# Optimization experiments

Measured on AMD Instinct MI355X. Metric: run time of the kernel, lower is better.

The kernel has to match this reference:

```python
import jax, jax.numpy as jnp
import numpy as np

N = 512     # nodes
E = 16384   # edges (N * avg_degree 32, unique pairs)
F = 64      # nedgeinput
FO = 64     # nedgeoutput


def setup_inputs() -> dict:
    key = jax.random.key(0)
    ks = jax.random.split(key, 7)
    # unique edge pairs so scatter-assign is well-defined
    perm = jax.random.permutation(ks[0], N * N)[:E]
    edge_index = jnp.stack([perm // N, perm % N]).astype(jnp.int32)  # [2, E]
    C = jax.random.normal(ks[1], (E, F), dtype=jnp.float32)
    batch_node = jax.random.normal(ks[2], (N,), dtype=jnp.float32)
    s = 1.0 / np.sqrt(F)
    W_L1 = jax.random.normal(ks[3], (F, F), dtype=jnp.float32) * s          # Linear(F, F), weight [out,in]
    W_L2 = jax.random.normal(ks[4], (F, F), dtype=jnp.float32) * s
    W_mlp1 = jax.random.normal(ks[5], (8 * F, 2 * F), dtype=jnp.float32) * (1.0 / np.sqrt(2 * F))
    W_mlp2 = jax.random.normal(ks[6], (FO, 8 * F), dtype=jnp.float32) * (1.0 / np.sqrt(8 * F))
    return {"edge_index": edge_index, "C": C, "batch_node": batch_node,
            "W_L1": W_L1, "W_L2": W_L2, "W_mlp1": W_mlp1, "W_mlp2": W_mlp2}


def reference(edge_index, C, batch_node, W_L1, W_L2, W_mlp1, W_mlp2):
    n = batch_node.shape[0]
    f = C.shape[1]
    ei0, ei1 = edge_index[0], edge_index[1]
    X = C @ W_L1.T  # [E, F]  (L1(C))
    Y = C @ W_L2.T  # [E, F]  (L2(C))
    # scatter edges into dense [F, N, N] adjacency-like tensors
    resx = jnp.zeros((f, n, n), dtype=C.dtype).at[:, ei0, ei1].set(X.T)
    resy = jnp.zeros((f, n, n), dtype=C.dtype).at[:, ei0, ei1].set(Y.T)
    # batched dense matmul per feature channel, then gather back at edges
    res = jnp.einsum('fij,fjk->fik', resx, resy)  # [F, N, N]
    tmp_matmul = res[:, ei0, ei1].T  # [E, F]
    tmp = jnp.concatenate([C, tmp_matmul], axis=1)  # [E, 2F]
    return jax.nn.relu(tmp @ W_mlp1.T) @ W_mlp2.T  # [E, FO]
```

## Files before the change

kernel.cpp:

```cpp
#include <hip/hip_runtime.h>

#define NN 512
#define NE 16384
#define NF 64

typedef __attribute__((ext_vector_type(8))) short short8_t;
typedef __attribute__((ext_vector_type(4))) float float4_t;

__device__ inline unsigned short f2bf(float f) {
  unsigned u = __builtin_bit_cast(unsigned, f);
  u += 0x7fff + ((u >> 16) & 1);
  return (unsigned short)(u >> 16);
}
__device__ inline float bf2f(unsigned short u) {
  unsigned v = ((unsigned)u) << 16;
  return __builtin_bit_cast(float, v);
}

__global__ __launch_bounds__(256) void k_xy_mfma(const float* __restrict__ C,
                                                 const float* __restrict__ W1,
                                                 const float* __restrict__ W2,
                                                 const int* __restrict__ ei,
                                                 const float* __restrict__ Wm1,
                                                 const float* __restrict__ Wm2,
                                                 int* __restrict__ eid,
                                                 unsigned* __restrict__ maskO,
                                                 unsigned* __restrict__ maskI,
                                                 unsigned short* __restrict__ Xb,
                                                 unsigned short* __restrict__ Yb,
                                                 unsigned short* __restrict__ W1B,
                                                 unsigned short* __restrict__ W2B) {
  __shared__ __attribute__((aligned(16))) short W1s[64 * 72];
  __shared__ __attribute__((aligned(16))) short W2s[64 * 72];
  int t = threadIdx.x;
  int w = t >> 6;
  int lane = t & 63;
  int col = lane & 15;
  int q = lane >> 4;
  int base_e = blockIdx.x * 64 + w * 16;

  if (t < 64) {
    int e = blockIdx.x * 64 + t;
    int i = ei[e];
    int k = ei[NE + e];
    eid[i * NN + k] = e;
    atomicOr(&maskO[i * 16 + (k >> 5)], 1u << (k & 31));
    atomicOr(&maskI[k * 16 + (i >> 5)], 1u << (i & 31));
  }

  if (t >= 64 && t < 160) {
    int t4 = blockIdx.x * 96 + (t - 64);
    if (t4 < 16384) {
      float4 v = ((const float4*)Wm1)[t4];
      short4 s;
      s.x = f2bf(v.x); s.y = f2bf(v.y); s.z = f2bf(v.z); s.w = f2bf(v.w);
      ((short4*)W1B)[t4] = s;
    } else {
      int i2 = t4 - 16384;
      float4 v = ((const float4*)Wm2)[i2];
      short4 s;
      s.x = f2bf(v.x); s.y = f2bf(v.y); s.z = f2bf(v.z); s.w = f2bf(v.w);
      ((short4*)W2B)[i2] = s;
    }
  }

#pragma unroll
  for (int z = 0; z < 4; z++) {
    int gi = z * 256 + t;
    int r = gi >> 4, c = gi & 15;
    float4 v1 = ((const float4*)W1)[r * 16 + c];
    float4 v2 = ((const float4*)W2)[r * 16 + c];
    short4 s1, s2;
    s1.x = f2bf(v1.x); s1.y = f2bf(v1.y); s1.z = f2bf(v1.z); s1.w = f2bf(v1.w);
    s2.x = f2bf(v2.x); s2.y = f2bf(v2.y); s2.z = f2bf(v2.z); s2.w = f2bf(v2.w);
    *(short4*)(W1s + r * 72 + c * 4) = s1;
    *(short4*)(W2s + r * 72 + c * 4) = s2;
  }
  __syncthreads();

  short8_t bfrag[2];
#pragma unroll
  for (int ks = 0; ks < 2; ks++) {
    float4 c0 = ((const float4*)C)[(size_t)(base_e + col) * 16 + ks * 8 + q * 2];
    float4 c1 = ((const float4*)C)[(size_t)(base_e + col) * 16 + ks * 8 + q * 2 + 1];
    short8_t s;
    s[0] = (short)f2bf(c0.x); s[1] = (short)f2bf(c0.y);
    s[2] = (short)f2bf(c0.z); s[3] = (short)f2bf(c0.w);
    s[4] = (short)f2bf(c1.x); s[5] = (short)f2bf(c1.y);
    s[6] = (short)f2bf(c1.z); s[7] = (short)f2bf(c1.w);
    bfrag[ks] = s;
  }

  float4_t xa[4], ya[4];
#pragma unroll
  for (int ft = 0; ft < 4; ft++) {
    xa[ft] = (float4_t){0.f, 0.f, 0.f, 0.f};
    ya[ft] = (float4_t){0.f, 0.f, 0.f, 0.f};
  }
#pragma unroll
  for (int ks = 0; ks < 2; ks++) {
#pragma unroll
    for (int ft = 0; ft < 4; ft++) {
      short8_t a1 = *(const short8_t*)(W1s + (ft * 16 + col) * 72 + ks * 32 + q * 8);
      short8_t a2 = *(const short8_t*)(W2s + (ft * 16 + col) * 72 + ks * 32 + q * 8);
      xa[ft] = __builtin_amdgcn_mfma_f32_16x16x32_bf16(a1, bfrag[ks], xa[ft], 0, 0, 0);
      ya[ft] = __builtin_amdgcn_mfma_f32_16x16x32_bf16(a2, bfrag[ks], ya[ft], 0, 0, 0);
    }
  }
#pragma unroll
  for (int ft = 0; ft < 4; ft++) {
    short4 sx, sy;
    sx.x = (short)f2bf(xa[ft][0]); sx.y = (short)f2bf(xa[ft][1]);
    sx.z = (short)f2bf(xa[ft][2]); sx.w = (short)f2bf(xa[ft][3]);
    sy.x = (short)f2bf(ya[ft][0]); sy.y = (short)f2bf(ya[ft][1]);
    sy.z = (short)f2bf(ya[ft][2]); sy.w = (short)f2bf(ya[ft][3]);
    *(short4*)(Xb + (size_t)(base_e + col) * 64 + ft * 16 + q * 4) = sx;
    *(short4*)(Yb + (size_t)(base_e + col) * 64 + ft * 16 + q * 4) = sy;
  }
}

#define STAGE(it) { \
    uint4* d1 = (uint4*)W1s; const uint4* s1g = (const uint4*)W1B; \
    _Pragma("unroll") for (int z = 0; z < 4; z++) { \
      int gi = z * 512 + t; int r = gi >> 4, c = gi & 15; \
      int grow = ((r >> 6) * 4 + (it)) * 64 + (r & 63); \
      d1[r * 17 + c] = s1g[(size_t)grow * 16 + c]; } \
    uint4* d2 = (uint4*)W2s; const uint4* s2g = (const uint4*)W2B; \
    _Pragma("unroll") for (int z = 0; z < 2; z++) { \
      int gi = z * 512 + t; int r = gi >> 4, c = gi & 15; \
      int gc = ((c >> 3) * 4 + (it)) * 8 + (c & 7); \
      d2[r * 17 + c] = s2g[(size_t)r * 64 + gc]; } }

#define REMBATCH(le, ii, kk, cnt, ac) { \
    int t2 = base + b; \
    int jj = jlbase[(le) * 32 + (t2 < (cnt) ? t2 : base)] & 511; \
    int sv = eid[(gl < 8) ? ((ii) * NN + jj) : (jj * NN + (kk))]; \
    short4 xs[8], ys[8]; \
    _Pragma("unroll") for (int b2 = 0; b2 < 8; b2++) { \
      int s1 = __shfl(sv, (lane & 48) | b2); \
      int s2 = __shfl(sv, (lane & 48) | (8 + b2)); \
      xs[b2] = *(const short4*)(Xb + (size_t)s1 * 64 + gl * 4); \
      ys[b2] = *(const short4*)(Yb + (size_t)s2 * 64 + gl * 4); } \
    _Pragma("unroll") for (int b2 = 0; b2 < 8; b2++) if (base + b2 < (cnt)) { \
      ac[0] = fmaf(bf2f((unsigned short)xs[b2].x), bf2f((unsigned short)ys[b2].x), ac[0]); \
      ac[1] = fmaf(bf2f((unsigned short)xs[b2].y), bf2f((unsigned short)ys[b2].y), ac[1]); \
      ac[2] = fmaf(bf2f((unsigned short)xs[b2].z), bf2f((unsigned short)ys[b2].z), ac[2]); \
      ac[3] = fmaf(bf2f((unsigned short)xs[b2].w), bf2f((unsigned short)ys[b2].w), ac[3]); } }

__global__ __launch_bounds__(512) void k_spmlp(
    const int* __restrict__ ei,
    const int* __restrict__ eid,
    const unsigned* __restrict__ maskO,
    const unsigned* __restrict__ maskI,
    const unsigned short* __restrict__ Xb,
    const unsigned short* __restrict__ Yb,
    const float* __restrict__ C,
    const unsigned short* __restrict__ W1B,
    const unsigned short* __restrict__ W2B,
    float* __restrict__ out) {
  __shared__ __attribute__((aligned(16))) short W1s[128 * 136];
  __shared__ __attribute__((aligned(16))) short W2s[64 * 136];
  __shared__ __attribute__((aligned(16))) short hS[8][16 * 72];
  __shared__ __attribute__((aligned(16))) short tm[64 * 72];

  int t = threadIdx.x;
  int w = t >> 6;
  int lane = t & 63;
  int gl = lane & 15;
  int grp = lane >> 4;
  unsigned short* jlbase = (unsigned short*)hS;

  int u = w >> 2;
  int wl = w & 3;
  int g = wl & 1;
  int h = wl >> 1;
  int col = lane & 15;
  int q = lane >> 4;
  int base_e = blockIdx.x * 64 + u * 32 + g * 16;
  int lem = u * 32 + g * 16 + col;

  int le0 = w * 4 + grp;
  int le1 = 32 + w * 4 + grp;
  int e0 = blockIdx.x * 64 + le0;
  int e1 = blockIdx.x * 64 + le1;
  int i0 = ei[e0], k0 = ei[NE + e0];
  int i1 = ei[e1], k1 = ei[NE + e1];

  float4 craw[4];
#pragma unroll
  for (int ks = 0; ks < 2; ks++) {
    craw[2 * ks]     = ((const float4*)C)[(size_t)(base_e + col) * 16 + ks * 8 + q * 2];
    craw[2 * ks + 1] = ((const float4*)C)[(size_t)(base_e + col) * 16 + ks * 8 + q * 2 + 1];
  }
  STAGE(0);

  unsigned mm0 = maskO[i0 * 16 + gl] & maskI[k0 * 16 + gl];
  unsigned mm1 = maskO[i1 * 16 + gl] & maskI[k1 * 16 + gl];

  int cnt0, cnt1;
#pragma unroll
  for (int round = 0; round < 2; round++) {
    unsigned mm = round ? mm1 : mm0;
    int le = round ? le1 : le0;
    int mcnt = __popc(mm);
    int incl = mcnt;
#pragma unroll
    for (int d = 1; d < 16; d <<= 1) {
      int y = __shfl(incl, (lane & 48) | ((gl - d) & 15));
      if (gl >= d) incl += y;
    }
    int off = incl - mcnt;
    int cnt = __shfl(incl, (lane & 48) | 15);
    unsigned bits = mm;
    while (bits) {
      int bb = __builtin_ctz(bits);
      bits &= bits - 1;
      if (off < 32) jlbase[le * 32 + off] = (unsigned short)(gl * 32 + bb);
      off++;
    }
    if (cnt > 32) cnt = 32;
    if (round) cnt1 = cnt; else cnt0 = cnt;
  }

  int b = gl & 7;
  float ac0[4] = {0.f, 0.f, 0.f, 0.f}, ac1[4] = {0.f, 0.f, 0.f, 0.f};
  {
    int jj0 = jlbase[le0 * 32 + (b < cnt0 ? b : 0)] & 511;
    int jj1 = jlbase[le1 * 32 + (b < cnt1 ? b : 0)] & 511;
    int sv0 = (cnt0 > 0) ? eid[(gl < 8) ? (i0 * NN + jj0) : (jj0 * NN + k0)] : 0;
    int sv1 = (cnt1 > 0) ? eid[(gl < 8) ? (i1 * NN + jj1) : (jj1 * NN + k1)] : 0;
    short4 xs0[8], ys0[8], xs1[8], ys1[8];
#pragma unroll
    for (int b2 = 0; b2 < 8; b2++) {
      int s1 = __shfl(sv0, (lane & 48) | b2);
      int s2 = __shfl(sv0, (lane & 48) | (8 + b2));
      xs0[b2] = *(const short4*)(Xb + (size_t)s1 * 64 + gl * 4);
      ys0[b2] = *(const short4*)(Yb + (size_t)s2 * 64 + gl * 4);
    }
#pragma unroll
    for (int b2 = 0; b2 < 8; b2++) {
      int s1 = __shfl(sv1, (lane & 48) | b2);
      int s2 = __shfl(sv1, (lane & 48) | (8 + b2));
      xs1[b2] = *(const short4*)(Xb + (size_t)s1 * 64 + gl * 4);
      ys1[b2] = *(const short4*)(Yb + (size_t)s2 * 64 + gl * 4);
    }
#pragma unroll
    for (int b2 = 0; b2 < 8; b2++) if (b2 < cnt0) {
      ac0[0] = fmaf(bf2f((unsigned short)xs0[b2].x), bf2f((unsigned short)ys0[b2].x), ac0[0]);
      ac0[1] = fmaf(bf2f((unsigned short)xs0[b2].y), bf2f((unsigned short)ys0[b2].y), ac0[1]);
      ac0[2] = fmaf(bf2f((unsigned short)xs0[b2].z), bf2f((unsigned short)ys0[b2].z), ac0[2]);
      ac0[3] = fmaf(bf2f((unsigned short)xs0[b2].w), bf2f((unsigned short)ys0[b2].w), ac0[3]);
    }
#pragma unroll
    for (int b2 = 0; b2 < 8; b2++) if (b2 < cnt1) {
      ac1[0] = fmaf(bf2f((unsigned short)xs1[b2].x), bf2f((unsigned short)ys1[b2].x), ac1[0]);
      ac1[1] = fmaf(bf2f((unsigned short)xs1[b2].y), bf2f((unsigned short)ys1[b2].y), ac1[1]);
      ac1[2] = fmaf(bf2f((unsigned short)xs1[b2].z), bf2f((unsigned short)ys1[b2].z), ac1[2]);
      ac1[3] = fmaf(bf2f((unsigned short)xs1[b2].w), bf2f((unsigned short)ys1[b2].w), ac1[3]);
    }
  }
  for (int base = 8; base < cnt0; base += 8) REMBATCH(le0, i0, k0, cnt0, ac0);
  for (int base = 8; base < cnt1; base += 8) REMBATCH(le1, i1, k1, cnt1, ac1);

  {
    short4 o0, o1;
    o0.x = (short)f2bf(ac0[0]); o0.y = (short)f2bf(ac0[1]);
    o0.z = (short)f2bf(ac0[2]); o0.w = (short)f2bf(ac0[3]);
    o1.x = (short)f2bf(ac1[0]); o1.y = (short)f2bf(ac1[1]);
    o1.z = (short)f2bf(ac1[2]); o1.w = (short)f2bf(ac1[3]);
    *(short4*)(tm + le0 * 72 + gl * 4) = o0;
    *(short4*)(tm + le1 * 72 + gl * 4) = o1;
  }

  __syncthreads();

  short8_t btmp[4];
#pragma unroll
  for (int ks = 0; ks < 2; ks++) {
    float4 c0 = craw[2 * ks], c1 = craw[2 * ks + 1];
    short8_t s;
    s[0] = (short)f2bf(c0.x); s[1] = (short)f2bf(c0.y);
    s[2] = (short)f2bf(c0.z); s[3] = (short)f2bf(c0.w);
    s[4] = (short)f2bf(c1.x); s[5] = (short)f2bf(c1.y);
    s[6] = (short)f2bf(c1.z); s[7] = (short)f2bf(c1.w);
    btmp[ks] = s;
  }
#pragma unroll
  for (int ks = 2; ks < 4; ks++)
    btmp[ks] = *(const short8_t*)(tm + lem * 72 + (ks - 2) * 32 + q * 8);

  float4_t oacc[4];
#pragma unroll
  for (int ft = 0; ft < 4; ft++) oacc[ft] = (float4_t){0.f, 0.f, 0.f, 0.f};

  for (int it = 0; it < 4; it++) {
#pragma unroll
    for (int ht = 0; ht < 4; ht++) {
      float4_t hacc = (float4_t){0.f, 0.f, 0.f, 0.f};
#pragma unroll
      for (int ks = 0; ks < 4; ks++) {
        short8_t af = *(const short8_t*)(W1s + (h * 64 + ht * 16 + col) * 136 + ks * 32 + q * 8);
        hacc = __builtin_amdgcn_mfma_f32_16x16x32_bf16(af, btmp[ks], hacc, 0, 0, 0);
      }
      short4 hp;
      hp.x = (short)f2bf(fmaxf(hacc[0], 0.f));
      hp.y = (short)f2bf(fmaxf(hacc[1], 0.f));
      hp.z = (short)f2bf(fmaxf(hacc[2], 0.f));
      hp.w = (short)f2bf(fmaxf(hacc[3], 0.f));
      *(short4*)(&hS[w][col * 72 + ht * 16 + q * 4]) = hp;
    }

#pragma unroll
    for (int ks2 = 0; ks2 < 2; ks2++) {
      short8_t a2 = *(const short8_t*)(&hS[w][col * 72 + ks2 * 32 + q * 8]);
#pragma unroll
      for (int ft = 0; ft < 4; ft++) {
        short8_t b2 = *(const short8_t*)(W2s + (ft * 16 + col) * 136 + h * 64 + ks2 * 32 + q * 8);
        oacc[ft] = __builtin_amdgcn_mfma_f32_16x16x32_bf16(a2, b2, oacc[ft], 0, 0, 0);
      }
    }

    if (it < 3) {
      __syncthreads();
      STAGE(it + 1);
      __syncthreads();
    }
  }

  __syncthreads();
  float* red = (float*)W1s;
  if (h == 1) {
#pragma unroll
    for (int ft = 0; ft < 4; ft++)
#pragma unroll
      for (int r = 0; r < 4; r++)
        red[(u * 32 + g * 16 + q * 4 + r) * 66 + ft * 16 + col] = oacc[ft][r];
  }
  __syncthreads();
  if (h == 0) {
#pragma unroll
    for (int ft = 0; ft < 4; ft++)
#pragma unroll
      for (int r = 0; r < 4; r++) {
        float v = oacc[ft][r] + red[(u * 32 + g * 16 + q * 4 + r) * 66 + ft * 16 + col];
        out[(size_t)(base_e + q * 4 + r) * 64 + ft * 16 + col] = v;
      }
  }
}

extern "C" void kernel_launch(void* const* d_in, const int* in_sizes, int n_in,
                              void* d_out, int out_size, void* d_ws, size_t ws_size,
                              hipStream_t stream) {
  const int* ei = (const int*)d_in[0];
  const float* C = (const float*)d_in[1];
  const float* W1 = (const float*)d_in[3];
  const float* W2 = (const float*)d_in[4];
  const float* Wm1 = (const float*)d_in[5];
  const float* Wm2 = (const float*)d_in[6];
  float* out = (float*)d_out;

  char* p = (char*)d_ws;
  int* eid = (int*)p;                 p += (size_t)NN * NN * 4;
  unsigned* masks = (unsigned*)p;     p += (size_t)16384 * 4;
  unsigned short* Xb = (unsigned short*)p;    p += (size_t)NE * NF * 2;
  unsigned short* Yb = (unsigned short*)p;    p += (size_t)NE * NF * 2;
  unsigned short* W1B = (unsigned short*)p;   p += (size_t)512 * 128 * 2;
  unsigned short* W2B = (unsigned short*)p;   p += (size_t)64 * 512 * 2;
  unsigned* maskO = masks;
  unsigned* maskI = masks + 8192;

  hipMemsetAsync(masks, 0, 16384 * sizeof(unsigned), stream);
  k_xy_mfma<<<NE / 64, 256, 0, stream>>>(C, W1, W2, ei, Wm1, Wm2, eid,
                                         maskO, maskI, Xb, Yb, W1B, W2B);
  k_spmlp<<<NE / 64, 512, 0, stream>>>(ei, eid, maskO, maskI, Xb, Yb,
                                       C, W1B, W2B, out);
}
```

Measured before the change: 88.34 us.

## Fuse projection and sparse-MLP kernels into one cooperative kernel with grid sync

Merges the X/Y projection kernel and the sparse matmul+MLP kernel into a single cooperative launch of 256 blocks, separated by a grid-wide barrier. The global memset and scattered global atomics for the adjacency bitmasks are replaced by two blocks that each build one full mask in shared memory with LDS atomics and then copy it out. This removes a kernel launch, the memset, and global atomic traffic. In exchange, two blocks serially scan all 16384 edges with 128 threads, which can lengthen the critical path before the grid sync. It also raises shared memory use and relies on all 256 blocks being co-resident.

```diff
diff --git a/kernel.cpp b/kernel.cpp
--- a/kernel.cpp
+++ b/kernel.cpp
@@ -1,8 +1,11 @@
 #include <hip/hip_runtime.h>
+#include <hip/hip_cooperative_groups.h>
 
 #define NN 512
 #define NE 16384
 #define NF 64
+
+namespace cg = cooperative_groups;
 
 typedef __attribute__((ext_vector_type(8))) short short8_t;
 typedef __attribute__((ext_vector_type(4))) float float4_t;
@@ -15,108 +18,6 @@
 __device__ inline float bf2f(unsigned short u) {
   unsigned v = ((unsigned)u) << 16;
   return __builtin_bit_cast(float, v);
-}
-
-__global__ __launch_bounds__(256) void k_xy_mfma(const float* __restrict__ C,
-                                                 const float* __restrict__ W1,
-                                                 const float* __restrict__ W2,
-                                                 const int* __restrict__ ei,
-                                                 const float* __restrict__ Wm1,
-                                                 const float* __restrict__ Wm2,
-                                                 int* __restrict__ eid,
-                                                 unsigned* __restrict__ maskO,
-                                                 unsigned* __restrict__ maskI,
-                                                 unsigned short* __restrict__ Xb,
-                                                 unsigned short* __restrict__ Yb,
-                                                 unsigned short* __restrict__ W1B,
-                                                 unsigned short* __restrict__ W2B) {
-  __shared__ __attribute__((aligned(16))) short W1s[64 * 72];
-  __shared__ __attribute__((aligned(16))) short W2s[64 * 72];
-  int t = threadIdx.x;
-  int w = t >> 6;
-  int lane = t & 63;
-  int col = lane & 15;
-  int q = lane >> 4;
-  int base_e = blockIdx.x * 64 + w * 16;
-
-  if (t < 64) {
-    int e = blockIdx.x * 64 + t;
-    int i = ei[e];
-    int k = ei[NE + e];
-    eid[i * NN + k] = e;
-    atomicOr(&maskO[i * 16 + (k >> 5)], 1u << (k & 31));
-    atomicOr(&maskI[k * 16 + (i >> 5)], 1u << (i & 31));
-  }
-
-  if (t >= 64 && t < 160) {
-    int t4 = blockIdx.x * 96 + (t - 64);
-    if (t4 < 16384) {
-      float4 v = ((const float4*)Wm1)[t4];
-      short4 s;
-      s.x = f2bf(v.x); s.y = f2bf(v.y); s.z = f2bf(v.z); s.w = f2bf(v.w);
-      ((short4*)W1B)[t4] = s;
-    } else {
-      int i2 = t4 - 16384;
-      float4 v = ((const float4*)Wm2)[i2];
-      short4 s;
-      s.x = f2bf(v.x); s.y = f2bf(v.y); s.z = f2bf(v.z); s.w = f2bf(v.w);
-      ((short4*)W2B)[i2] = s;
-    }
-  }
-
-#pragma unroll
-  for (int z = 0; z < 4; z++) {
-    int gi = z * 256 + t;
-    int r = gi >> 4, c = gi & 15;
-    float4 v1 = ((const float4*)W1)[r * 16 + c];
-    float4 v2 = ((const float4*)W2)[r * 16 + c];
-    short4 s1, s2;
-    s1.x = f2bf(v1.x); s1.y = f2bf(v1.y); s1.z = f2bf(v1.z); s1.w = f2bf(v1.w);
-    s2.x = f2bf(v2.x); s2.y = f2bf(v2.y); s2.z = f2bf(v2.z); s2.w = f2bf(v2.w);
-    *(short4*)(W1s + r * 72 + c * 4) = s1;
-    *(short4*)(W2s + r * 72 + c * 4) = s2;
-  }
-  __syncthreads();
-
-  short8_t bfrag[2];
-#pragma unroll
-  for (int ks = 0; ks < 2; ks++) {
-    float4 c0 = ((const float4*)C)[(size_t)(base_e + col) * 16 + ks * 8 + q * 2];
-    float4 c1 = ((const float4*)C)[(size_t)(base_e + col) * 16 + ks * 8 + q * 2 + 1];
-    short8_t s;
-    s[0] = (short)f2bf(c0.x); s[1] = (short)f2bf(c0.y);
-    s[2] = (short)f2bf(c0.z); s[3] = (short)f2bf(c0.w);
-    s[4] = (short)f2bf(c1.x); s[5] = (short)f2bf(c1.y);
-    s[6] = (short)f2bf(c1.z); s[7] = (short)f2bf(c1.w);
-    bfrag[ks] = s;
-  }
-
-  float4_t xa[4], ya[4];
-#pragma unroll
-  for (int ft = 0; ft < 4; ft++) {
-    xa[ft] = (float4_t){0.f, 0.f, 0.f, 0.f};
-    ya[ft] = (float4_t){0.f, 0.f, 0.f, 0.f};
-  }
-#pragma unroll
-  for (int ks = 0; ks < 2; ks++) {
-#pragma unroll
-    for (int ft = 0; ft < 4; ft++) {
-      short8_t a1 = *(const short8_t*)(W1s + (ft * 16 + col) * 72 + ks * 32 + q * 8);
-      short8_t a2 = *(const short8_t*)(W2s + (ft * 16 + col) * 72 + ks * 32 + q * 8);
-      xa[ft] = __builtin_amdgcn_mfma_f32_16x16x32_bf16(a1, bfrag[ks], xa[ft], 0, 0, 0);
-      ya[ft] = __builtin_amdgcn_mfma_f32_16x16x32_bf16(a2, bfrag[ks], ya[ft], 0, 0, 0);
-    }
-  }
-#pragma unroll
-  for (int ft = 0; ft < 4; ft++) {
-    short4 sx, sy;
-    sx.x = (short)f2bf(xa[ft][0]); sx.y = (short)f2bf(xa[ft][1]);
-    sx.z = (short)f2bf(xa[ft][2]); sx.w = (short)f2bf(xa[ft][3]);
-    sy.x = (short)f2bf(ya[ft][0]); sy.y = (short)f2bf(ya[ft][1]);
-    sy.z = (short)f2bf(ya[ft][2]); sy.w = (short)f2bf(ya[ft][3]);
-    *(short4*)(Xb + (size_t)(base_e + col) * 64 + ft * 16 + q * 4) = sx;
-    *(short4*)(Yb + (size_t)(base_e + col) * 64 + ft * 16 + q * 4) = sy;
-  }
 }
 
 #define STAGE(it) { \
@@ -147,21 +48,26 @@
       ac[2] = fmaf(bf2f((unsigned short)xs[b2].z), bf2f((unsigned short)ys[b2].z), ac[2]); \
       ac[3] = fmaf(bf2f((unsigned short)xs[b2].w), bf2f((unsigned short)ys[b2].w), ac[3]); } }
 
-__global__ __launch_bounds__(512) void k_spmlp(
+__global__ __launch_bounds__(512) void k_mega(
     const int* __restrict__ ei,
-    const int* __restrict__ eid,
-    const unsigned* __restrict__ maskO,
-    const unsigned* __restrict__ maskI,
-    const unsigned short* __restrict__ Xb,
-    const unsigned short* __restrict__ Yb,
     const float* __restrict__ C,
-    const unsigned short* __restrict__ W1B,
-    const unsigned short* __restrict__ W2B,
+    const float* __restrict__ W1,
+    const float* __restrict__ W2,
+    const float* __restrict__ Wm1,
+    const float* __restrict__ Wm2,
+    int* __restrict__ eid,
+    unsigned* __restrict__ maskO,
+    unsigned* __restrict__ maskI,
+    unsigned short* __restrict__ Xb,
+    unsigned short* __restrict__ Yb,
+    unsigned short* __restrict__ W1B,
+    unsigned short* __restrict__ W2B,
     float* __restrict__ out) {
   __shared__ __attribute__((aligned(16))) short W1s[128 * 136];
   __shared__ __attribute__((aligned(16))) short W2s[64 * 136];
   __shared__ __attribute__((aligned(16))) short hS[8][16 * 72];
   __shared__ __attribute__((aligned(16))) short tm[64 * 72];
+  __shared__ unsigned mlds[8192];
 
   int t = threadIdx.x;
   int w = t >> 6;
@@ -169,6 +75,8 @@
   int gl = lane & 15;
   int grp = lane >> 4;
   unsigned short* jlbase = (unsigned short*)hS;
+  short* k1W1s = &hS[0][0];
+  short* k1W2s = k1W1s + 64 * 72;
 
   int u = w >> 2;
   int wl = w & 3;
@@ -192,6 +100,112 @@
     craw[2 * ks]     = ((const float4*)C)[(size_t)(base_e + col) * 16 + ks * 8 + q * 2];
     craw[2 * ks + 1] = ((const float4*)C)[(size_t)(base_e + col) * 16 + ks * 8 + q * 2 + 1];
   }
+
+  if (blockIdx.x < 2) {
+    uint4 z4 = {0u, 0u, 0u, 0u};
+#pragma unroll
+    for (int z = 0; z < 4; z++) ((uint4*)mlds)[t * 4 + z] = z4;
+  }
+
+  if (t < 256) {
+#pragma unroll
+    for (int z = 0; z < 4; z++) {
+      int gi = z * 256 + t;
+      int r = gi >> 4, c = gi & 15;
+      float4 v1 = ((const float4*)W1)[r * 16 + c];
+      float4 v2 = ((const float4*)W2)[r * 16 + c];
+      short4 s1, s2;
+      s1.x = f2bf(v1.x); s1.y = f2bf(v1.y); s1.z = f2bf(v1.z); s1.w = f2bf(v1.w);
+      s2.x = f2bf(v2.x); s2.y = f2bf(v2.y); s2.z = f2bf(v2.z); s2.w = f2bf(v2.w);
+      *(short4*)(k1W1s + r * 72 + c * 4) = s1;
+      *(short4*)(k1W2s + r * 72 + c * 4) = s2;
+    }
+  } else if (t < 352) {
+    int t4 = blockIdx.x * 96 + (t - 256);
+    if (t4 < 16384) {
+      float4 v = ((const float4*)Wm1)[t4];
+      short4 s;
+      s.x = f2bf(v.x); s.y = f2bf(v.y); s.z = f2bf(v.z); s.w = f2bf(v.w);
+      ((short4*)W1B)[t4] = s;
+    } else {
+      int i2 = t4 - 16384;
+      float4 v = ((const float4*)Wm2)[i2];
+      short4 s;
+      s.x = f2bf(v.x); s.y = f2bf(v.y); s.z = f2bf(v.z); s.w = f2bf(v.w);
+      ((short4*)W2B)[i2] = s;
+    }
+  }
+
+  if (t < 64) {
+    int e = blockIdx.x * 64 + t;
+    eid[ei[e] * NN + ei[NE + e]] = e;
+  }
+
+  __syncthreads();
+
+  if (t < 256) {
+    int be = blockIdx.x * 64 + w * 16;
+    short8_t bfrag[2];
+#pragma unroll
+    for (int ks = 0; ks < 2; ks++) {
+      float4 c0 = ((const float4*)C)[(size_t)(be + col) * 16 + ks * 8 + q * 2];
+      float4 c1 = ((const float4*)C)[(size_t)(be + col) * 16 + ks * 8 + q * 2 + 1];
+      short8_t s;
+      s[0] = (short)f2bf(c0.x); s[1] = (short)f2bf(c0.y);
+      s[2] = (short)f2bf(c0.z); s[3] = (short)f2bf(c0.w);
+      s[4] = (short)f2bf(c1.x); s[5] = (short)f2bf(c1.y);
+      s[6] = (short)f2bf(c1.z); s[7] = (short)f2bf(c1.w);
+      bfrag[ks] = s;
+    }
+    float4_t xa[4], ya[4];
+#pragma unroll
+    for (int ft = 0; ft < 4; ft++) {
+      xa[ft] = (float4_t){0.f, 0.f, 0.f, 0.f};
+      ya[ft] = (float4_t){0.f, 0.f, 0.f, 0.f};
+    }
+#pragma unroll
+    for (int ks = 0; ks < 2; ks++) {
+#pragma unroll
+      for (int ft = 0; ft < 4; ft++) {
+        short8_t a1 = *(const short8_t*)(k1W1s + (ft * 16 + col) * 72 + ks * 32 + q * 8);
+        short8_t a2 = *(const short8_t*)(k1W2s + (ft * 16 + col) * 72 + ks * 32 + q * 8);
+        xa[ft] = __builtin_amdgcn_mfma_f32_16x16x32_bf16(a1, bfrag[ks], xa[ft], 0, 0, 0);
+        ya[ft] = __builtin_amdgcn_mfma_f32_16x16x32_bf16(a2, bfrag[ks], ya[ft], 0, 0, 0);
+      }
+    }
+#pragma unroll
+    for (int ft = 0; ft < 4; ft++) {
+      short4 sx, sy;
+      sx.x = (short)f2bf(xa[ft][0]); sx.y = (short)f2bf(xa[ft][1]);
+      sx.z = (short)f2bf(xa[ft][2]); sx.w = (short)f2bf(xa[ft][3]);
+      sy.x = (short)f2bf(ya[ft][0]); sy.y = (short)f2bf(ya[ft][1]);
+      sy.z = (short)f2bf(ya[ft][2]); sy.w = (short)f2bf(ya[ft][3]);
+      *(short4*)(Xb + (size_t)(be + col) * 64 + ft * 16 + q * 4) = sx;
+      *(short4*)(Yb + (size_t)(be + col) * 64 + ft * 16 + q * 4) = sy;
+    }
+  } else if (t >= 384 && blockIdx.x == 0) {
+    for (int e = t - 384; e < NE; e += 128) {
+      int ii = ei[e], kk = ei[NE + e];
+      atomicOr(&mlds[ii * 16 + (kk >> 5)], 1u << (kk & 31));
+    }
+  } else if (t >= 384 && blockIdx.x == 1) {
+    for (int e = t - 384; e < NE; e += 128) {
+      int ii = ei[e], kk = ei[NE + e];
+      atomicOr(&mlds[kk * 16 + (ii >> 5)], 1u << (ii & 31));
+    }
+  }
+
+  if (blockIdx.x < 2) {
+    __syncthreads();
+    unsigned* dst = (blockIdx.x == 0) ? maskO : maskI;
+#pragma unroll
+    for (int z = 0; z < 4; z++)
+      ((uint4*)dst)[t * 4 + z] = ((const uint4*)mlds)[t * 4 + z];
+  }
+
+  __threadfence();
+  cg::this_grid().sync();
+
   STAGE(0);
 
   unsigned mm0 = maskO[i0 * 16 + gl] & maskI[k0 * 16 + gl];
@@ -369,9 +383,10 @@
   unsigned* maskO = masks;
   unsigned* maskI = masks + 8192;
 
-  hipMemsetAsync(masks, 0, 16384 * sizeof(unsigned), stream);
-  k_xy_mfma<<<NE / 64, 256, 0, stream>>>(C, W1, W2, ei, Wm1, Wm2, eid,
-                                         maskO, maskI, Xb, Yb, W1B, W2B);
-  k_spmlp<<<NE / 64, 512, 0, stream>>>(ei, eid, maskO, maskI, Xb, Yb,
-                                       C, W1B, W2B, out);
+  void* args[] = {(void*)&ei, (void*)&C, (void*)&W1, (void*)&W2,
+                  (void*)&Wm1, (void*)&Wm2, (void*)&eid, (void*)&maskO,
+                  (void*)&maskI, (void*)&Xb, (void*)&Yb, (void*)&W1B,
+                  (void*)&W2B, (void*)&out};
+  hipLaunchCooperativeKernel((const void*)k_mega, dim3(256), dim3(512),
+                             args, 0, stream);
 }
```

New measurement: 218.3 us. +147.1%, slower.

## Double-buffer MLP weight staging and split X/Y projection across more blocks

Applied to the files above, without the earlier changes.

The MLP kernel now holds its weight tiles in two LDS buffers. The next slice is loaded into registers before compute and written to the other buffer afterwards, so global weight loads overlap the MFMA work and each iteration needs one barrier instead of two. The projection kernel gives each wave either X or Y for 16 edges and launches twice as many blocks with 32 edges each, hoisting the C loads to the top. Double buffering doubles the weight LDS footprint, which may reduce occupancy.

```diff
diff --git a/kernel.cpp b/kernel.cpp
--- a/kernel.cpp
+++ b/kernel.cpp
@@ -37,10 +37,19 @@
   int lane = t & 63;
   int col = lane & 15;
   int q = lane >> 4;
-  int base_e = blockIdx.x * 64 + w * 16;
-
-  if (t < 64) {
-    int e = blockIdx.x * 64 + t;
+  int p = w >> 1;
+  int xy = w & 1;
+  int base_e = blockIdx.x * 32 + p * 16;
+
+  float4 c0[2], c1[2];
+#pragma unroll
+  for (int ks = 0; ks < 2; ks++) {
+    c0[ks] = ((const float4*)C)[(size_t)(base_e + col) * 16 + ks * 8 + q * 2];
+    c1[ks] = ((const float4*)C)[(size_t)(base_e + col) * 16 + ks * 8 + q * 2 + 1];
+  }
+
+  if (t < 32) {
+    int e = blockIdx.x * 32 + t;
     int i = ei[e];
     int k = ei[NE + e];
     eid[i * NN + k] = e;
@@ -48,8 +57,8 @@
     atomicOr(&maskI[k * 16 + (i >> 5)], 1u << (i & 31));
   }
 
-  if (t >= 64 && t < 160) {
-    int t4 = blockIdx.x * 96 + (t - 64);
+  if (t >= 64 && t < 112) {
+    int t4 = blockIdx.x * 48 + (t - 64);
     if (t4 < 16384) {
       float4 v = ((const float4*)Wm1)[t4];
       short4 s;
@@ -81,55 +90,57 @@
   short8_t bfrag[2];
 #pragma unroll
   for (int ks = 0; ks < 2; ks++) {
-    float4 c0 = ((const float4*)C)[(size_t)(base_e + col) * 16 + ks * 8 + q * 2];
-    float4 c1 = ((const float4*)C)[(size_t)(base_e + col) * 16 + ks * 8 + q * 2 + 1];
     short8_t s;
-    s[0] = (short)f2bf(c0.x); s[1] = (short)f2bf(c0.y);
-    s[2] = (short)f2bf(c0.z); s[3] = (short)f2bf(c0.w);
-    s[4] = (short)f2bf(c1.x); s[5] = (short)f2bf(c1.y);
-    s[6] = (short)f2bf(c1.z); s[7] = (short)f2bf(c1.w);
+    s[0] = (short)f2bf(c0[ks].x); s[1] = (short)f2bf(c0[ks].y);
+    s[2] = (short)f2bf(c0[ks].z); s[3] = (short)f2bf(c0[ks].w);
+    s[4] = (short)f2bf(c1[ks].x); s[5] = (short)f2bf(c1[ks].y);
+    s[6] = (short)f2bf(c1[ks].z); s[7] = (short)f2bf(c1[ks].w);
     bfrag[ks] = s;
   }
 
-  float4_t xa[4], ya[4];
+  const short* Ws = xy ? W2s : W1s;
+  unsigned short* Ob = xy ? Yb : Xb;
+  float4_t acc[4];
+#pragma unroll
+  for (int ft = 0; ft < 4; ft++) acc[ft] = (float4_t){0.f, 0.f, 0.f, 0.f};
+#pragma unroll
+  for (int ks = 0; ks < 2; ks++) {
+#pragma unroll
+    for (int ft = 0; ft < 4; ft++) {
+      short8_t a = *(const short8_t*)(Ws + (ft * 16 + col) * 72 + ks * 32 + q * 8);
+      acc[ft] = __builtin_amdgcn_mfma_f32_16x16x32_bf16(a, bfrag[ks], acc[ft], 0, 0, 0);
+    }
+  }
 #pragma unroll
   for (int ft = 0; ft < 4; ft++) {
-    xa[ft] = (float4_t){0.f, 0.f, 0.f, 0.f};
-    ya[ft] = (float4_t){0.f, 0.f, 0.f, 0.f};
-  }
-#pragma unroll
-  for (int ks = 0; ks < 2; ks++) {
-#pragma unroll
-    for (int ft = 0; ft < 4; ft++) {
-      short8_t a1 = *(const short8_t*)(W1s + (ft * 16 + col) * 72 + ks * 32 + q * 8);
-      short8_t a2 = *(const short8_t*)(W2s + (ft * 16 + col) * 72 + ks * 32 + q * 8);
-      xa[ft] = __builtin_amdgcn_mfma_f32_16x16x32_bf16(a1, bfrag[ks], xa[ft], 0, 0, 0);
-      ya[ft] = __builtin_amdgcn_mfma_f32_16x16x32_bf16(a2, bfrag[ks], ya[ft], 0, 0, 0);
-    }
-  }
-#pragma unroll
-  for (int ft = 0; ft < 4; ft++) {
-    short4 sx, sy;
-    sx.x = (short)f2bf(xa[ft][0]); sx.y = (short)f2bf(xa[ft][1]);
-    sx.z = (short)f2bf(xa[ft][2]); sx.w = (short)f2bf(xa[ft][3]);
-    sy.x = (short)f2bf(ya[ft][0]); sy.y = (short)f2bf(ya[ft][1]);
-    sy.z = (short)f2bf(ya[ft][2]); sy.w = (short)f2bf(ya[ft][3]);
-    *(short4*)(Xb + (size_t)(base_e + col) * 64 + ft * 16 + q * 4) = sx;
-    *(short4*)(Yb + (size_t)(base_e + col) * 64 + ft * 16 + q * 4) = sy;
-  }
-}
-
-#define STAGE(it) { \
-    uint4* d1 = (uint4*)W1s; const uint4* s1g = (const uint4*)W1B; \
+    short4 so;
+    so.x = (short)f2bf(acc[ft][0]); so.y = (short)f2bf(acc[ft][1]);
+    so.z = (short)f2bf(acc[ft][2]); so.w = (short)f2bf(acc[ft][3]);
+    *(short4*)(Ob + (size_t)(base_e + col) * 64 + ft * 16 + q * 4) = so;
+  }
+}
+
+#define STAGE_LOAD(it, r1, r2) { \
+    const uint4* s1g = (const uint4*)W1B; \
     _Pragma("unroll") for (int z = 0; z < 4; z++) { \
       int gi = z * 512 + t; int r = gi >> 4, c = gi & 15; \
       int grow = ((r >> 6) * 4 + (it)) * 64 + (r & 63); \
-      d1[r * 17 + c] = s1g[(size_t)grow * 16 + c]; } \
-    uint4* d2 = (uint4*)W2s; const uint4* s2g = (const uint4*)W2B; \
+      r1[z] = s1g[(size_t)grow * 16 + c]; } \
+    const uint4* s2g = (const uint4*)W2B; \
     _Pragma("unroll") for (int z = 0; z < 2; z++) { \
       int gi = z * 512 + t; int r = gi >> 4, c = gi & 15; \
       int gc = ((c >> 3) * 4 + (it)) * 8 + (c & 7); \
-      d2[r * 17 + c] = s2g[(size_t)r * 64 + gc]; } }
+      r2[z] = s2g[(size_t)r * 64 + gc]; } }
+
+#define STAGE_WRITE(buf, r1, r2) { \
+    uint4* d1 = (uint4*)(W1s[(buf)]); \
+    _Pragma("unroll") for (int z = 0; z < 4; z++) { \
+      int gi = z * 512 + t; int r = gi >> 4, c = gi & 15; \
+      d1[r * 17 + c] = r1[z]; } \
+    uint4* d2 = (uint4*)(W2s[(buf)]); \
+    _Pragma("unroll") for (int z = 0; z < 2; z++) { \
+      int gi = z * 512 + t; int r = gi >> 4, c = gi & 15; \
+      d2[r * 17 + c] = r2[z]; } }
 
 #define REMBATCH(le, ii, kk, cnt, ac) { \
     int t2 = base + b; \
@@ -158,8 +169,8 @@
     const unsigned short* __restrict__ W1B,
     const unsigned short* __restrict__ W2B,
     float* __restrict__ out) {
-  __shared__ __attribute__((aligned(16))) short W1s[128 * 136];
-  __shared__ __attribute__((aligned(16))) short W2s[64 * 136];
+  __shared__ __attribute__((aligned(16))) short W1s[2][128 * 136];
+  __shared__ __attribute__((aligned(16))) short W2s[2][64 * 136];
   __shared__ __attribute__((aligned(16))) short hS[8][16 * 72];
   __shared__ __attribute__((aligned(16))) short tm[64 * 72];
 
@@ -192,10 +203,12 @@
     craw[2 * ks]     = ((const float4*)C)[(size_t)(base_e + col) * 16 + ks * 8 + q * 2];
     craw[2 * ks + 1] = ((const float4*)C)[(size_t)(base_e + col) * 16 + ks * 8 + q * 2 + 1];
   }
-  STAGE(0);
+  uint4 sr1[4], sr2[2];
+  STAGE_LOAD(0, sr1, sr2);
 
   unsigned mm0 = maskO[i0 * 16 + gl] & maskI[k0 * 16 + gl];
   unsigned mm1 = maskO[i1 * 16 + gl] & maskI[k1 * 16 + gl];
+  STAGE_WRITE(0, sr1, sr2);
 
   int cnt0, cnt1;
 #pragma unroll
@@ -277,12 +290,12 @@
   short8_t btmp[4];
 #pragma unroll
   for (int ks = 0; ks < 2; ks++) {
-    float4 c0 = craw[2 * ks], c1 = craw[2 * ks + 1];
+    float4 f0 = craw[2 * ks], f1 = craw[2 * ks + 1];
     short8_t s;
-    s[0] = (short)f2bf(c0.x); s[1] = (short)f2bf(c0.y);
-    s[2] = (short)f2bf(c0.z); s[3] = (short)f2bf(c0.w);
-    s[4] = (short)f2bf(c1.x); s[5] = (short)f2bf(c1.y);
-    s[6] = (short)f2bf(c1.z); s[7] = (short)f2bf(c1.w);
+    s[0] = (short)f2bf(f0.x); s[1] = (short)f2bf(f0.y);
+    s[2] = (short)f2bf(f0.z); s[3] = (short)f2bf(f0.w);
+    s[4] = (short)f2bf(f1.x); s[5] = (short)f2bf(f1.y);
+    s[6] = (short)f2bf(f1.z); s[7] = (short)f2bf(f1.w);
     btmp[ks] = s;
   }
 #pragma unroll
@@ -294,12 +307,16 @@
   for (int ft = 0; ft < 4; ft++) oacc[ft] = (float4_t){0.f, 0.f, 0.f, 0.f};
 
   for (int it = 0; it < 4; it++) {
+    if (it < 3) STAGE_LOAD(it + 1, sr1, sr2);
+    const short* W1c = W1s[it & 1];
+    const short* W2c = W2s[it & 1];
+
 #pragma unroll
     for (int ht = 0; ht < 4; ht++) {
       float4_t hacc = (float4_t){0.f, 0.f, 0.f, 0.f};
 #pragma unroll
       for (int ks = 0; ks < 4; ks++) {
-        short8_t af = *(const short8_t*)(W1s + (h * 64 + ht * 16 + col) * 136 + ks * 32 + q * 8);
+        short8_t af = *(const short8_t*)(W1c + (h * 64 + ht * 16 + col) * 136 + ks * 32 + q * 8);
         hacc = __builtin_amdgcn_mfma_f32_16x16x32_bf16(af, btmp[ks], hacc, 0, 0, 0);
       }
       short4 hp;
@@ -315,19 +332,15 @@
       short8_t a2 = *(const short8_t*)(&hS[w][col * 72 + ks2 * 32 + q * 8]);
 #pragma unroll
       for (int ft = 0; ft < 4; ft++) {
-        short8_t b2 = *(const short8_t*)(W2s + (ft * 16 + col) * 136 + h * 64 + ks2 * 32 + q * 8);
+        short8_t b2 = *(const short8_t*)(W2c + (ft * 16 + col) * 136 + h * 64 + ks2 * 32 + q * 8);
         oacc[ft] = __builtin_amdgcn_mfma_f32_16x16x32_bf16(a2, b2, oacc[ft], 0, 0, 0);
       }
     }
 
-    if (it < 3) {
-      __syncthreads();
-      STAGE(it + 1);
-      __syncthreads();
-    }
-  }
-
-  __syncthreads();
+    if (it < 3) STAGE_WRITE((it + 1) & 1, sr1, sr2);
+    __syncthreads();
+  }
+
   float* red = (float*)W1s;
   if (h == 1) {
 #pragma unroll
@@ -370,7 +383,7 @@
   unsigned* maskI = masks + 8192;
 
   hipMemsetAsync(masks, 0, 16384 * sizeof(unsigned), stream);
-  k_xy_mfma<<<NE / 64, 256, 0, stream>>>(C, W1, W2, ei, Wm1, Wm2, eid,
+  k_xy_mfma<<<NE / 32, 256, 0, stream>>>(C, W1, W2, ei, Wm1, Wm2, eid,
                                          maskO, maskI, Xb, Yb, W1B, W2B);
   k_spmlp<<<NE / 64, 512, 0, stream>>>(ei, eid, maskO, maskI, Xb, Yb,
                                        C, W1B, W2B, out);
```

Result: no change. 88.30 us (-0.0%).
